# Kernel optimization log

Hardware: AMD Instinct MI355X
Metric: run time of the kernel (lower is better)

Reference implementation:

```python
import jax, jax.numpy as jnp
import numpy as np

INPUT_SIZE = 8
WINDOW = 128
HIDDEN = 256
B, T = 1024, 256

def _cell(W_ih, W_hh, b_ih, b_hh, h, c, x):
    # PyTorch LSTM gate order: i, f, g, o
    gates = x @ W_ih.T + h @ W_hh.T + b_ih + b_hh  # [B, 4H]
    i, f, g, o = jnp.split(gates, 4, axis=-1)
    c = jax.nn.sigmoid(f) * c + jax.nn.sigmoid(i) * jnp.tanh(g)
    h = jax.nn.sigmoid(o) * jnp.tanh(c)
    return h, c

def setup_inputs() -> dict:
    key = jax.random.key(0)
    ks = jax.random.split(key, 12)
    s = 1.0 / np.sqrt(HIDDEN)
    u = lambda k, shape: jax.random.uniform(k, shape, jnp.float32, -s, s)
    return {
        'x': jax.random.normal(ks[0], (B, T, INPUT_SIZE), jnp.float32),
        'W_ih0': u(ks[1], (4 * HIDDEN, INPUT_SIZE)),
        'W_hh0': u(ks[2], (4 * HIDDEN, HIDDEN)),
        'b_ih0': u(ks[3], (4 * HIDDEN,)),
        'b_hh0': u(ks[4], (4 * HIDDEN,)),
        'W_ih1': u(ks[5], (4 * HIDDEN, HIDDEN)),
        'W_hh1': u(ks[6], (4 * HIDDEN, HIDDEN)),
        'b_ih1': u(ks[7], (4 * HIDDEN,)),
        'b_hh1': u(ks[8], (4 * HIDDEN,)),
        'W_lin': u(ks[9], (1, HIDDEN)),
        'b_lin': u(ks[10], (1,)),
    }

def reference(x, W_ih0, W_hh0, b_ih0, b_hh0, W_ih1, W_hh1, b_ih1, b_hh1, W_lin, b_lin):
    Bx = x.shape[0]
    h0 = jnp.zeros((Bx, HIDDEN), x.dtype)
    params = [(W_ih0, W_hh0, b_ih0, b_hh0), (W_ih1, W_hh1, b_ih1, b_hh1)]

    # ---- warmup: multi-layer LSTM over first WINDOW steps ----
    x_pre = jnp.swapaxes(x[:, :WINDOW], 0, 1)   # [W, B, in]
    x_post = jnp.swapaxes(x[:, WINDOW:, 1:], 0, 1)  # [T-W, B, in-1]

    hs, cs = [], []
    seq = x_pre
    for (Wi, Wh, bi, bh) in params:
        def step(carry, xt, Wi=Wi, Wh=Wh, bi=bi, bh=bh):
            h, c = carry
            h, c = _cell(Wi, Wh, bi, bh, h, c, xt)
            return (h, c), h
        (hT, cT), seq = jax.lax.scan(step, (h0, h0), seq)
        hs.append(hT); cs.append(cT)

    pred0 = hs[-1] @ W_lin.T + b_lin  # [B, 1]

    def ar_step(carry, xt_rest):
        h0_, c0_, h1_, c1_, pred = carry
        xin = jnp.concatenate([pred, xt_rest], axis=1)  # [B, in]
        h0_, c0_ = _cell(W_ih0, W_hh0, b_ih0, b_hh0, h0_, c0_, xin)
        h1_, c1_ = _cell(W_ih1, W_hh1, b_ih1, b_hh1, h1_, c1_, h0_)
        pred = h1_ @ W_lin.T + b_lin
        return (h0_, c0_, h1_, c1_, pred), pred

    carry0 = (hs[0], cs[0], hs[1], cs[1], pred0)
    _, preds = jax.lax.scan(ar_step, carry0, x_post)  # [T-W, B, 1]

    out = jnp.concatenate([pred0[None], preds], axis=0)  # [T-W+1, B, 1]
    return jnp.swapaxes(out, 0, 1)  # [B, T-W+1, 1]
```

## Files before the change

kernel.cpp:

```cpp
#include <hip/hip_runtime.h>
#include <cstdint>

#define HID 256
#define TT 256
#define WIN 128
#define OUTW 129
#define NBLK 64
#define ROWS 16
#define NTHR 1024
#define NKK 25
#define NE (NKK * 64 * 512)

typedef _Float16 half8 __attribute__((ext_vector_type(8)));
typedef _Float16 half4 __attribute__((ext_vector_type(4)));
typedef float f32x4 __attribute__((ext_vector_type(4)));
typedef int i32x4 __attribute__((ext_vector_type(4)));

#define ALO  4.8828125e-4f
#define SLOC 1.5018521e-8f

__device__ __forceinline__ float sigm(float z)  { return 1.0f / (1.0f + __expf(-z)); }
__device__ __forceinline__ float tanhx(float z) { float e = __expf(2.0f * z); return 1.0f - 2.0f / (e + 1.0f); }

__device__ __forceinline__ void split_f(float v, _Float16& hi, _Float16& lo) {
  float h = (fabsf(v) < 0.0009765625f) ? 0.0f : (float)(_Float16)v;
  hi = (_Float16)h;
  lo = (_Float16)((v - h) * 2048.0f);
}
__device__ __forceinline__ signed char q8(float v) {
  return (signed char)__float2int_rn(fminf(fmaxf(v * 32.0f, -127.0f), 127.0f));
}

__global__ void prep_pack(const float* __restrict__ Wih0, const float* __restrict__ Whh0,
                          const float* __restrict__ Wih1, const float* __restrict__ Whh1,
                          _Float16* __restrict__ wpH, signed char* __restrict__ wpI) {
  for (int e = blockIdx.x * blockDim.x + threadIdx.x; e < NE; e += gridDim.x * blockDim.x) {
    const int kkG = e >> 15;
    const int nt = (e >> 9) & 63, l = (e >> 3) & 63, j = e & 7;
    const int kl = ((l >> 4) << 3) + j;
    const int n  = (nt << 4) + (l & 15);
    float w;
    if (kkG == 0)     w = (kl < 8) ? Wih0[n * 8 + kl] : 0.0f;
    else if (kkG < 9) w = Whh0[n * 256 + (kkG - 1) * 32 + kl];
    else {
      const int k = (kkG - 9) * 32 + kl;
      w = (k < 256) ? Wih1[n * 256 + k] : Whh1[n * 256 + (k - 256)];
    }
    const float hi = (fabsf(w) < 6.103515625e-5f) ? 0.0f : (float)(_Float16)w;
    wpH[e] = (_Float16)hi;
    int q = __float2int_rn((w - hi) * 2080768.0f);
    q = q > 127 ? 127 : (q < -127 ? -127 : q);
    wpI[e] = (signed char)q;
  }
}

__device__ __forceinline__ void mfma_kk(
    const _Float16* __restrict__ wpH, const signed char* __restrict__ wpI,
    int kkG, int w, int lane,
    const _Float16* __restrict__ ahp, const _Float16* __restrict__ alp,
    const signed char* __restrict__ aip,
    f32x4 (&accM)[4], f32x4 (&accA)[4], i32x4 (&accI)[4])
{
  const half8 ah = *(const half8*)ahp;
  const half8 al = *(const half8*)alp;
  const long  a8 = *(const long*)aip;
  const size_t b0 = ((size_t)kkG * 64 + w) * 512 + (size_t)lane * 8;
  #pragma unroll
  for (int i = 0; i < 4; ++i) {
    const half8 bh = *(const half8*)(wpH + b0 + (size_t)(i << 4) * 512);
    const long  b8 = *(const long*)(wpI + b0 + (size_t)(i << 4) * 512);
    accM[i] = __builtin_amdgcn_mfma_f32_16x16x32_f16(ah, bh, accM[i], 0, 0, 0);
    accA[i] = __builtin_amdgcn_mfma_f32_16x16x32_f16(al, bh, accA[i], 0, 0, 0);
    accI[i] = __builtin_amdgcn_mfma_i32_16x16x32_i8(a8, b8, accI[i], 0, 0, 0);
  }
}

__device__ __forceinline__ void epi(
    f32x4 (&accM)[4], f32x4 (&accA)[4], i32x4 (&accI)[4],
    float bi, float bf, float bg, float bo, float (&cst)[4],
    _Float16* __restrict__ Ah, _Float16* __restrict__ Al, signed char* __restrict__ Ai,
    int e0)
{
  #pragma unroll
  for (int q = 0; q < 4; ++q) {
    const float gi = accM[0][q] + ALO * accA[0][q] + SLOC * (float)accI[0][q] + bi;
    const float gf = accM[1][q] + ALO * accA[1][q] + SLOC * (float)accI[1][q] + bf;
    const float gg = accM[2][q] + ALO * accA[2][q] + SLOC * (float)accI[2][q] + bg;
    const float go = accM[3][q] + ALO * accA[3][q] + SLOC * (float)accI[3][q] + bo;
    const float c = sigm(gf) * cst[q] + sigm(gi) * tanhx(gg);
    cst[q] = c;
    const float h = sigm(go) * tanhx(c);
    _Float16 hh, hl; split_f(h, hh, hl);
    const int idx = e0 + (q << 3);
    Ah[idx] = hh; Al[idx] = hl; Ai[idx] = q8(h);
  }
}

__global__ __launch_bounds__(NTHR, 4) void lstm_mfma(
    const float* __restrict__ x,
    const float* __restrict__ bih0, const float* __restrict__ bhh0,
    const float* __restrict__ bih1, const float* __restrict__ bhh1,
    const float* __restrict__ Wlin, const float* __restrict__ blin,
    const _Float16* __restrict__ wpH, const signed char* __restrict__ wpI,
    float* __restrict__ out)
{
  __shared__ __align__(16) _Float16 A1h[8192];
  __shared__ __align__(16) _Float16 A1l[8192];
  __shared__ __align__(16) signed char A1i[8192];
  __shared__ __align__(16) _Float16 A0xh[512];
  __shared__ __align__(16) _Float16 A0xl[512];
  __shared__ __align__(16) signed char A0xi[512];
  __shared__ __align__(16) float sWlin[256];

  const int tid = threadIdx.x, lane = tid & 63, w = tid >> 6;
  const int r0 = blockIdx.x * ROWS;
  const int u = (w << 4) + (lane & 15);
  const int e0 = (((u >> 5) << 6) + (((u >> 3) & 3) << 4) + (((lane >> 4)) << 2)) * 8 + (u & 7);

  for (int i = tid; i < 8192; i += NTHR) { A1h[i] = (_Float16)0.f; A1l[i] = (_Float16)0.f; A1i[i] = 0; }
  if (tid < 512) { A0xh[tid] = (_Float16)0.f; A0xl[tid] = (_Float16)0.f; A0xi[tid] = 0; }
  if (tid < 256) sWlin[tid] = Wlin[tid];

  const float b0i = bih0[u]       + bhh0[u];
  const float b0f = bih0[u + 256] + bhh0[u + 256];
  const float b0g = bih0[u + 512] + bhh0[u + 512];
  const float b0o = bih0[u + 768] + bhh0[u + 768];
  const float b1i = bih1[u]       + bhh1[u];
  const float b1f = bih1[u + 256] + bhh1[u + 256];
  const float b1g = bih1[u + 512] + bhh1[u + 512];
  const float b1o = bih1[u + 768] + bhh1[u + 768];
  const float blv = blin[0];
  float c0[4] = {0.f, 0.f, 0.f, 0.f}, c1[4] = {0.f, 0.f, 0.f, 0.f};
  __syncthreads();

  for (int t = 0; t < TT; ++t) {
    if (t >= WIN) {
      const int u0 = lane << 2;
      const int pb = ((8 + (u0 >> 5)) * 64 + (((u0 >> 3) & 3) << 4) + w) * 8 + (u0 & 7);
      const half4 h4 = *(const half4*)(A1h + pb);
      const half4 l4 = *(const half4*)(A1l + pb);
      const float4 wl = *(const float4*)(sWlin + u0);
      float s = wl.x * ((float)h4.x + ALO * (float)l4.x)
              + wl.y * ((float)h4.y + ALO * (float)l4.y)
              + wl.z * ((float)h4.z + ALO * (float)l4.z)
              + wl.w * ((float)h4.w + ALO * (float)l4.w);
      #pragma unroll
      for (int m = 1; m < 64; m <<= 1) s += __shfl_xor(s, m);
      if (lane == 0) {
        const float pv = s + blv;
        out[(size_t)(r0 + w) * OUTW + (t - WIN)] = pv;
        _Float16 hh, hl; split_f(pv, hh, hl);
        A0xh[w << 3] = hh; A0xl[w << 3] = hl; A0xi[w << 3] = q8(pv);
      }
    }
    if (tid < 128) {
      const int r = tid >> 3, f = tid & 7;
      if (f > 0 || t < WIN) {
        const float v = x[((size_t)(r0 + r) * TT + t) * 8 + f];
        _Float16 hh, hl; split_f(v, hh, hl);
        A0xh[(r << 3) + f] = hh; A0xl[(r << 3) + f] = hl; A0xi[(r << 3) + f] = q8(v);
      }
    }
    __syncthreads();

    {
      f32x4 z4 = {0.f, 0.f, 0.f, 0.f}; i32x4 zi = {0, 0, 0, 0};
      f32x4 accM[4] = {z4, z4, z4, z4}, accA[4] = {z4, z4, z4, z4};
      i32x4 accI[4] = {zi, zi, zi, zi};
      mfma_kk(wpH, wpI, 0, w, lane,
              A0xh + lane * 8, A0xl + lane * 8, A0xi + lane * 8, accM, accA, accI);
      #pragma unroll 4
      for (int c = 1; c < 9; ++c) {
        const int ao = ((c - 1) * 64 + lane) * 8;
        mfma_kk(wpH, wpI, c, w, lane, A1h + ao, A1l + ao, A1i + ao, accM, accA, accI);
      }
      __syncthreads();
      epi(accM, accA, accI, b0i, b0f, b0g, b0o, c0, A1h, A1l, A1i, e0);
    }
    __syncthreads();

    {
      f32x4 z4 = {0.f, 0.f, 0.f, 0.f}; i32x4 zi = {0, 0, 0, 0};
      f32x4 accM[4] = {z4, z4, z4, z4}, accA[4] = {z4, z4, z4, z4};
      i32x4 accI[4] = {zi, zi, zi, zi};
      #pragma unroll 4
      for (int c = 0; c < 16; ++c) {
        const int ao = (c * 64 + lane) * 8;
        mfma_kk(wpH, wpI, 9 + c, w, lane, A1h + ao, A1l + ao, A1i + ao, accM, accA, accI);
      }
      __syncthreads();
      epi(accM, accA, accI, b1i, b1f, b1g, b1o, c1, A1h + 4096, A1l + 4096, A1i + 4096, e0);
    }
    __syncthreads();
  }

  {
    const int u0 = lane << 2;
    const int pb = ((8 + (u0 >> 5)) * 64 + (((u0 >> 3) & 3) << 4) + w) * 8 + (u0 & 7);
    const half4 h4 = *(const half4*)(A1h + pb);
    const half4 l4 = *(const half4*)(A1l + pb);
    const float4 wl = *(const float4*)(sWlin + u0);
    float s = wl.x * ((float)h4.x + ALO * (float)l4.x)
            + wl.y * ((float)h4.y + ALO * (float)l4.y)
            + wl.z * ((float)h4.z + ALO * (float)l4.z)
            + wl.w * ((float)h4.w + ALO * (float)l4.w);
    #pragma unroll
    for (int m = 1; m < 64; m <<= 1) s += __shfl_xor(s, m);
    if (lane == 0) out[(size_t)(r0 + w) * OUTW + 128] = s + blv;
  }
}

extern "C" void kernel_launch(void* const* d_in, const int* in_sizes, int n_in,
                              void* d_out, int out_size, void* d_ws, size_t ws_size,
                              hipStream_t stream) {
  (void)in_sizes; (void)n_in; (void)out_size; (void)ws_size;
  const float* x    = (const float*)d_in[0];
  const float* Wih0 = (const float*)d_in[1];
  const float* Whh0 = (const float*)d_in[2];
  const float* bih0 = (const float*)d_in[3];
  const float* bhh0 = (const float*)d_in[4];
  const float* Wih1 = (const float*)d_in[5];
  const float* Whh1 = (const float*)d_in[6];
  const float* bih1 = (const float*)d_in[7];
  const float* bhh1 = (const float*)d_in[8];
  const float* Wlin = (const float*)d_in[9];
  const float* blin = (const float*)d_in[10];
  _Float16* wpH   = (_Float16*)d_ws;
  signed char* wpI = (signed char*)d_ws + (size_t)NE * 2;
  float* out = (float*)d_out;

  prep_pack<<<1600, 256, 0, stream>>>(Wih0, Whh0, Wih1, Whh1, wpH, wpI);
  lstm_mfma<<<NBLK, NTHR, 0, stream>>>(x, bih0, bhh0, bih1, bhh1,
                                       Wlin, blin, wpH, wpI, out);
}
```

Measured before the change: 12.25 ms.

## Stream packed weights into LDS with async global_load_lds double buffering

Each step's weight tiles, which were loaded straight from global memory into registers, are now staged through a two-slot LDS buffer using global_load_lds. Manual vmcnt and lgkmcnt waits let the next unit's prefetch overlap the current MFMAs, and a continuous unit schedule runs across both layers and timesteps. The int8 residual weights are repacked so each lane reads two tiles' worth in one 16-byte load. The kernel now needs about 140KB of dynamic LDS and relies on hand-counted waitcnt, which is fragile if the compiler reorders memory operations.

```diff
diff --git a/kernel.cpp b/kernel.cpp
--- a/kernel.cpp
+++ b/kernel.cpp
@@ -10,14 +10,33 @@
 #define NTHR 1024
 #define NKK 25
 #define NE (NKK * 64 * 512)
+#define NP (NKK * 32 * 64 * 16)
 
 typedef _Float16 half8 __attribute__((ext_vector_type(8)));
 typedef _Float16 half4 __attribute__((ext_vector_type(4)));
 typedef float f32x4 __attribute__((ext_vector_type(4)));
 typedef int i32x4 __attribute__((ext_vector_type(4)));
+typedef long l2v __attribute__((ext_vector_type(2)));
 
 #define ALO  4.8828125e-4f
 #define SLOC 1.5018521e-8f
+
+#define B_HALF   49152
+#define OFF_A1H  98304
+#define OFF_A1L  114688
+#define OFF_A1I  131072
+#define OFF_A0XH 139264
+#define OFF_A0XL 140288
+#define OFF_A0XI 141312
+#define OFF_WLIN 141824
+#define SMEM_BYTES 142848
+
+#define VMWAIT3() asm volatile("s_waitcnt vmcnt(3)" ::: "memory")
+#define LGKM0()   asm volatile("s_waitcnt lgkmcnt(0)" ::: "memory")
+#define BAR()     { LGKM0(); __builtin_amdgcn_s_barrier(); asm volatile("" ::: "memory"); }
+
+#define MF16(a,b,c) __builtin_amdgcn_mfma_f32_16x16x32_f16(a,b,c,0,0,0)
+#define MI8(a,b,c)  __builtin_amdgcn_mfma_i32_16x16x32_i8(a,b,c,0,0,0)
 
 __device__ __forceinline__ float sigm(float z)  { return 1.0f / (1.0f + __expf(-z)); }
 __device__ __forceinline__ float tanhx(float z) { float e = __expf(2.0f * z); return 1.0f - 2.0f / (e + 1.0f); }
@@ -31,48 +50,64 @@
   return (signed char)__float2int_rn(fminf(fmaxf(v * 32.0f, -127.0f), 127.0f));
 }
 
+__device__ __forceinline__ void gload16(const void* g, void* l) {
+  __builtin_amdgcn_global_load_lds(
+      (const __attribute__((address_space(1))) void*)g,
+      (__attribute__((address_space(3))) void*)l, 16, 0, 0);
+}
+
+__device__ __forceinline__ float fetch_w(int kkG, int kl, int n,
+    const float* __restrict__ Wih0, const float* __restrict__ Whh0,
+    const float* __restrict__ Wih1, const float* __restrict__ Whh1) {
+  if (kkG == 0) return (kl < 8) ? Wih0[n * 8 + kl] : 0.0f;
+  if (kkG < 9)  return Whh0[n * 256 + (kkG - 1) * 32 + kl];
+  const int k = (kkG - 9) * 32 + kl;
+  return (k < 256) ? Wih1[n * 256 + k] : Whh1[n * 256 + (k - 256)];
+}
+
 __global__ void prep_pack(const float* __restrict__ Wih0, const float* __restrict__ Whh0,
                           const float* __restrict__ Wih1, const float* __restrict__ Whh1,
-                          _Float16* __restrict__ wpH, signed char* __restrict__ wpI) {
-  for (int e = blockIdx.x * blockDim.x + threadIdx.x; e < NE; e += gridDim.x * blockDim.x) {
+                          _Float16* __restrict__ wpH, unsigned char* __restrict__ wpP) {
+  const int stride = gridDim.x * blockDim.x;
+  for (int e = blockIdx.x * blockDim.x + threadIdx.x; e < NE; e += stride) {
     const int kkG = e >> 15;
     const int nt = (e >> 9) & 63, l = (e >> 3) & 63, j = e & 7;
     const int kl = ((l >> 4) << 3) + j;
     const int n  = (nt << 4) + (l & 15);
-    float w;
-    if (kkG == 0)     w = (kl < 8) ? Wih0[n * 8 + kl] : 0.0f;
-    else if (kkG < 9) w = Whh0[n * 256 + (kkG - 1) * 32 + kl];
-    else {
-      const int k = (kkG - 9) * 32 + kl;
-      w = (k < 256) ? Wih1[n * 256 + k] : Whh1[n * 256 + (k - 256)];
-    }
+    const float w = fetch_w(kkG, kl, n, Wih0, Whh0, Wih1, Whh1);
     const float hi = (fabsf(w) < 6.103515625e-5f) ? 0.0f : (float)(_Float16)w;
     wpH[e] = (_Float16)hi;
+  }
+  for (int e = blockIdx.x * blockDim.x + threadIdx.x; e < NP; e += stride) {
+    const int kkG = e >> 15;
+    const int rem = e & 32767;
+    const int pair = rem >> 10;
+    const int l = (rem >> 4) & 63;
+    const int b = rem & 15;
+    const int tilesel = b >> 3, j = b & 7;
+    const int nt = ((pair >> 4) << 5) + (pair & 15) + (tilesel << 4);
+    const int kl = ((l >> 4) << 3) + j;
+    const int n  = (nt << 4) + (l & 15);
+    const float w = fetch_w(kkG, kl, n, Wih0, Whh0, Wih1, Whh1);
+    const float hi = (fabsf(w) < 6.103515625e-5f) ? 0.0f : (float)(_Float16)w;
     int q = __float2int_rn((w - hi) * 2080768.0f);
     q = q > 127 ? 127 : (q < -127 ? -127 : q);
-    wpI[e] = (signed char)q;
-  }
-}
-
-__device__ __forceinline__ void mfma_kk(
-    const _Float16* __restrict__ wpH, const signed char* __restrict__ wpI,
-    int kkG, int w, int lane,
-    const _Float16* __restrict__ ahp, const _Float16* __restrict__ alp,
-    const signed char* __restrict__ aip,
-    f32x4 (&accM)[4], f32x4 (&accA)[4], i32x4 (&accI)[4])
-{
-  const half8 ah = *(const half8*)ahp;
-  const half8 al = *(const half8*)alp;
-  const long  a8 = *(const long*)aip;
-  const size_t b0 = ((size_t)kkG * 64 + w) * 512 + (size_t)lane * 8;
-  #pragma unroll
-  for (int i = 0; i < 4; ++i) {
-    const half8 bh = *(const half8*)(wpH + b0 + (size_t)(i << 4) * 512);
-    const long  b8 = *(const long*)(wpI + b0 + (size_t)(i << 4) * 512);
-    accM[i] = __builtin_amdgcn_mfma_f32_16x16x32_f16(ah, bh, accM[i], 0, 0, 0);
-    accA[i] = __builtin_amdgcn_mfma_f32_16x16x32_f16(al, bh, accA[i], 0, 0, 0);
-    accI[i] = __builtin_amdgcn_mfma_i32_16x16x32_i8(a8, b8, accI[i], 0, 0, 0);
-  }
+    wpP[e] = (unsigned char)(signed char)q;
+  }
+}
+
+__device__ __forceinline__ void stage_unit(int u, int w, int lane,
+    const _Float16* __restrict__ wpH, const unsigned char* __restrict__ wpP,
+    char* __restrict__ sB) {
+  const int kkG  = (u < 18) ? (u >> 1) : (9 + ((u - 18) >> 1));
+  const int half = u & 1;
+  const int nt0  = (half << 5) + w;
+  char* dst = sB + (half ? B_HALF : 0) + w * 3072;
+  const char* sH0 = (const char*)(wpH + (((size_t)(kkG << 6) + nt0) << 9)) + (lane << 4);
+  const char* sP  = (const char*)wpP + (((size_t)(kkG << 5) + (half << 4) + w) << 10) + (lane << 4);
+  gload16(sH0,          dst);
+  gload16(sH0 + 16384,  dst + 1024);
+  gload16(sP,           dst + 2048);
 }
 
 __device__ __forceinline__ void epi(
@@ -101,21 +136,23 @@
     const float* __restrict__ bih0, const float* __restrict__ bhh0,
     const float* __restrict__ bih1, const float* __restrict__ bhh1,
     const float* __restrict__ Wlin, const float* __restrict__ blin,
-    const _Float16* __restrict__ wpH, const signed char* __restrict__ wpI,
+    const _Float16* __restrict__ wpH, const unsigned char* __restrict__ wpP,
     float* __restrict__ out)
 {
-  __shared__ __align__(16) _Float16 A1h[8192];
-  __shared__ __align__(16) _Float16 A1l[8192];
-  __shared__ __align__(16) signed char A1i[8192];
-  __shared__ __align__(16) _Float16 A0xh[512];
-  __shared__ __align__(16) _Float16 A0xl[512];
-  __shared__ __align__(16) signed char A0xi[512];
-  __shared__ __align__(16) float sWlin[256];
+  extern __shared__ char sm[];
+  char* sB = sm;
+  _Float16*    A1h  = (_Float16*)(sm + OFF_A1H);
+  _Float16*    A1l  = (_Float16*)(sm + OFF_A1L);
+  signed char* A1i  = (signed char*)(sm + OFF_A1I);
+  _Float16*    A0xh = (_Float16*)(sm + OFF_A0XH);
+  _Float16*    A0xl = (_Float16*)(sm + OFF_A0XL);
+  signed char* A0xi = (signed char*)(sm + OFF_A0XI);
+  float*       sWlin = (float*)(sm + OFF_WLIN);
 
   const int tid = threadIdx.x, lane = tid & 63, w = tid >> 6;
   const int r0 = blockIdx.x * ROWS;
   const int u = (w << 4) + (lane & 15);
-  const int e0 = (((u >> 5) << 6) + (((u >> 3) & 3) << 4) + (((lane >> 4)) << 2)) * 8 + (u & 7);
+  const int e0 = (((u >> 5) << 6) + (((u >> 3) & 3) << 4) + ((lane >> 4) << 2)) * 8 + (u & 7);
 
   for (int i = tid; i < 8192; i += NTHR) { A1h[i] = (_Float16)0.f; A1l[i] = (_Float16)0.f; A1i[i] = 0; }
   if (tid < 512) { A0xh[tid] = (_Float16)0.f; A0xl[tid] = (_Float16)0.f; A0xi[tid] = 0; }
@@ -131,7 +168,10 @@
   const float b1o = bih1[u + 768] + bhh1[u + 768];
   const float blv = blin[0];
   float c0[4] = {0.f, 0.f, 0.f, 0.f}, c1[4] = {0.f, 0.f, 0.f, 0.f};
-  __syncthreads();
+  BAR();
+
+  stage_unit(0, w, lane, wpH, wpP, sB);
+  stage_unit(1, w, lane, wpH, wpP, sB);
 
   for (int t = 0; t < TT; ++t) {
     if (t >= WIN) {
@@ -161,37 +201,93 @@
         A0xh[(r << 3) + f] = hh; A0xl[(r << 3) + f] = hl; A0xi[(r << 3) + f] = q8(v);
       }
     }
-    __syncthreads();
+    BAR();
 
     {
       f32x4 z4 = {0.f, 0.f, 0.f, 0.f}; i32x4 zi = {0, 0, 0, 0};
       f32x4 accM[4] = {z4, z4, z4, z4}, accA[4] = {z4, z4, z4, z4};
       i32x4 accI[4] = {zi, zi, zi, zi};
-      mfma_kk(wpH, wpI, 0, w, lane,
-              A0xh + lane * 8, A0xl + lane * 8, A0xi + lane * 8, accM, accA, accI);
-      #pragma unroll 4
-      for (int c = 1; c < 9; ++c) {
-        const int ao = ((c - 1) * 64 + lane) * 8;
-        mfma_kk(wpH, wpI, c, w, lane, A1h + ao, A1l + ao, A1i + ao, accM, accA, accI);
+      half8 ah, al; long a8;
+      #pragma unroll
+      for (int c = 0; c < 9; ++c) {
+        {
+          const char* mb = sB + w * 3072;
+          VMWAIT3();
+          const half8 bh0 = *(const half8*)(mb + (lane << 4));
+          const half8 bh1 = *(const half8*)(mb + 1024 + (lane << 4));
+          const l2v pp    = *(const l2v*)(mb + 2048 + (lane << 4));
+          if (c == 0) {
+            ah = *(const half8*)(A0xh + (lane << 3));
+            al = *(const half8*)(A0xl + (lane << 3));
+            a8 = *(const long*)(A0xi + (lane << 3));
+          } else {
+            const int ao = (((c - 1) << 6) + lane) << 3;
+            ah = *(const half8*)(A1h + ao);
+            al = *(const half8*)(A1l + ao);
+            a8 = *(const long*)(A1i + ao);
+          }
+          LGKM0();
+          stage_unit(2 * c + 2, w, lane, wpH, wpP, sB);
+          accM[0] = MF16(ah, bh0, accM[0]); accA[0] = MF16(al, bh0, accA[0]); accI[0] = MI8(a8, pp[0], accI[0]);
+          accM[1] = MF16(ah, bh1, accM[1]); accA[1] = MF16(al, bh1, accA[1]); accI[1] = MI8(a8, pp[1], accI[1]);
+        }
+        {
+          const char* mb = sB + B_HALF + w * 3072;
+          VMWAIT3();
+          const half8 bh0 = *(const half8*)(mb + (lane << 4));
+          const half8 bh1 = *(const half8*)(mb + 1024 + (lane << 4));
+          const l2v pp    = *(const l2v*)(mb + 2048 + (lane << 4));
+          LGKM0();
+          stage_unit(2 * c + 3, w, lane, wpH, wpP, sB);
+          accM[2] = MF16(ah, bh0, accM[2]); accA[2] = MF16(al, bh0, accA[2]); accI[2] = MI8(a8, pp[0], accI[2]);
+          accM[3] = MF16(ah, bh1, accM[3]); accA[3] = MF16(al, bh1, accA[3]); accI[3] = MI8(a8, pp[1], accI[3]);
+        }
       }
-      __syncthreads();
+      BAR();
       epi(accM, accA, accI, b0i, b0f, b0g, b0o, c0, A1h, A1l, A1i, e0);
     }
-    __syncthreads();
+    BAR();
 
     {
       f32x4 z4 = {0.f, 0.f, 0.f, 0.f}; i32x4 zi = {0, 0, 0, 0};
       f32x4 accM[4] = {z4, z4, z4, z4}, accA[4] = {z4, z4, z4, z4};
       i32x4 accI[4] = {zi, zi, zi, zi};
-      #pragma unroll 4
+      half8 ah, al; long a8;
+      #pragma unroll
       for (int c = 0; c < 16; ++c) {
-        const int ao = (c * 64 + lane) * 8;
-        mfma_kk(wpH, wpI, 9 + c, w, lane, A1h + ao, A1l + ao, A1i + ao, accM, accA, accI);
+        {
+          const char* mb = sB + w * 3072;
+          VMWAIT3();
+          const half8 bh0 = *(const half8*)(mb + (lane << 4));
+          const half8 bh1 = *(const half8*)(mb + 1024 + (lane << 4));
+          const l2v pp    = *(const l2v*)(mb + 2048 + (lane << 4));
+          const int ao = ((c << 6) + lane) << 3;
+          ah = *(const half8*)(A1h + ao);
+          al = *(const half8*)(A1l + ao);
+          a8 = *(const long*)(A1i + ao);
+          LGKM0();
+          const int uu = (20 + 2 * c >= 50) ? (20 + 2 * c - 50) : (20 + 2 * c);
+          stage_unit(uu, w, lane, wpH, wpP, sB);
+          accM[0] = MF16(ah, bh0, accM[0]); accA[0] = MF16(al, bh0, accA[0]); accI[0] = MI8(a8, pp[0], accI[0]);
+          accM[1] = MF16(ah, bh1, accM[1]); accA[1] = MF16(al, bh1, accA[1]); accI[1] = MI8(a8, pp[1], accI[1]);
+        }
+        {
+          const char* mb = sB + B_HALF + w * 3072;
+          VMWAIT3();
+          const half8 bh0 = *(const half8*)(mb + (lane << 4));
+          const half8 bh1 = *(const half8*)(mb + 1024 + (lane << 4));
+          const l2v pp    = *(const l2v*)(mb + 2048 + (lane << 4));
+          LGKM0();
+          const int uu = (21 + 2 * c >= 50) ? (21 + 2 * c - 50) : (21 + 2 * c);
+          stage_unit(uu, w, lane, wpH, wpP, sB);
+          accM[2] = MF16(ah, bh0, accM[2]); accA[2] = MF16(al, bh0, accA[2]); accI[2] = MI8(a8, pp[0], accI[2]);
+          accM[3] = MF16(ah, bh1, accM[3]); accA[3] = MF16(al, bh1, accA[3]); accI[3] = MI8(a8, pp[1], accI[3]);
+        }
       }
-      __syncthreads();
+      BAR();
       epi(accM, accA, accI, b1i, b1f, b1g, b1o, c1, A1h + 4096, A1l + 4096, A1i + 4096, e0);
     }
-    __syncthreads();
+    BAR();
   }
 
   {
@@ -225,11 +321,14 @@
   const float* bhh1 = (const float*)d_in[8];
   const float* Wlin = (const float*)d_in[9];
   const float* blin = (const float*)d_in[10];
-  _Float16* wpH   = (_Float16*)d_ws;
-  signed char* wpI = (signed char*)d_ws + (size_t)NE * 2;
+  _Float16* wpH     = (_Float16*)d_ws;
+  unsigned char* wpP = (unsigned char*)d_ws + (size_t)NE * 2;
   float* out = (float*)d_out;
 
-  prep_pack<<<1600, 256, 0, stream>>>(Wih0, Whh0, Wih1, Whh1, wpH, wpI);
-  lstm_mfma<<<NBLK, NTHR, 0, stream>>>(x, bih0, bhh0, bih1, bhh1,
-                                       Wlin, blin, wpH, wpI, out);
-}
+  prep_pack<<<1600, 256, 0, stream>>>(Wih0, Whh0, Wih1, Whh1, wpH, wpP);
+
+  (void)hipFuncSetAttribute(reinterpret_cast<const void*>(lstm_mfma),
+                            hipFuncAttributeMaxDynamicSharedMemorySize, SMEM_BYTES);
+  lstm_mfma<<<NBLK, NTHR, SMEM_BYTES, stream>>>(x, bih0, bhh0, bih1, bhh1,
+                                                Wlin, blin, wpH, wpP, out);
+}
```

Result: slower. 18.09 ms (+47.7%).

## Replace fp16 split-precision MFMA with multi-plane int8 MFMA emulation

Applied to the files above, without the earlier changes.

Switches the recurrent matmuls from fp16 hi/lo plus int8 correction MFMAs to a pure int8 scheme: weights are split into two int8 planes and hidden states into three int8 planes, combined with five i8 MFMAs per tile and scaled in the epilogue. The input projection for layer 0 (8 features) moves out of the MFMA path into per-thread fp32 FMAs using register-held weights, dropping one K-chunk. The final hidden state is also kept in fp32 shared memory for the linear head. This targets the higher throughput and smaller operand footprint of int8 MFMA, but raises the MFMA count per tile and may affect accuracy through the quantization.

```diff
diff --git a/kernel.cpp b/kernel.cpp
--- a/kernel.cpp
+++ b/kernel.cpp
@@ -8,202 +8,233 @@
 #define NBLK 64
 #define ROWS 16
 #define NTHR 1024
-#define NKK 25
-#define NE (NKK * 64 * 512)
-
-typedef _Float16 half8 __attribute__((ext_vector_type(8)));
-typedef _Float16 half4 __attribute__((ext_vector_type(4)));
+#define NKK 24
+#define PLANE_B (NKK * 32 * 64 * 16)
+
 typedef float f32x4 __attribute__((ext_vector_type(4)));
 typedef int i32x4 __attribute__((ext_vector_type(4)));
-
-#define ALO  4.8828125e-4f
-#define SLOC 1.5018521e-8f
+typedef long l2v __attribute__((ext_vector_type(2)));
+
+#define S1Q  4.9212598e-4f
+#define S0C  3.8750078e-6f
+#define C1   3.93700787e-3f
+#define C2   1.55000310e-5f
+#define R127 7.874015748e-3f
+#define R32258 3.10000620e-5f
+
+#define MI8(a,b,c) __builtin_amdgcn_mfma_i32_16x16x32_i8(a,b,c,0,0,0)
 
 __device__ __forceinline__ float sigm(float z)  { return 1.0f / (1.0f + __expf(-z)); }
 __device__ __forceinline__ float tanhx(float z) { float e = __expf(2.0f * z); return 1.0f - 2.0f / (e + 1.0f); }
 
-__device__ __forceinline__ void split_f(float v, _Float16& hi, _Float16& lo) {
-  float h = (fabsf(v) < 0.0009765625f) ? 0.0f : (float)(_Float16)v;
-  hi = (_Float16)h;
-  lo = (_Float16)((v - h) * 2048.0f);
-}
-__device__ __forceinline__ signed char q8(float v) {
-  return (signed char)__float2int_rn(fminf(fmaxf(v * 32.0f, -127.0f), 127.0f));
-}
-
-__global__ void prep_pack(const float* __restrict__ Wih0, const float* __restrict__ Whh0,
-                          const float* __restrict__ Wih1, const float* __restrict__ Whh1,
-                          _Float16* __restrict__ wpH, signed char* __restrict__ wpI) {
-  for (int e = blockIdx.x * blockDim.x + threadIdx.x; e < NE; e += gridDim.x * blockDim.x) {
+__device__ __forceinline__ int clamp127(int v) { return v > 127 ? 127 : (v < -127 ? -127 : v); }
+
+__device__ __forceinline__ void enc_h(float h, signed char& qh, signed char& ql, signed char& qll) {
+  float e = h;
+  int a = __float2int_rn(e * 127.0f);
+  e = fmaf((float)(-a), R127, e);
+  int b = clamp127(__float2int_rn(e * 32258.0f));
+  e = fmaf((float)(-b), R32258, e);
+  int c = clamp127(__float2int_rn(e * 8193532.0f));
+  qh = (signed char)a; ql = (signed char)b; qll = (signed char)c;
+}
+
+__global__ void prep_pack(const float* __restrict__ Whh0, const float* __restrict__ Wih1,
+                          const float* __restrict__ Whh1,
+                          signed char* __restrict__ wpHi, signed char* __restrict__ wpLo) {
+  const int stride = gridDim.x * blockDim.x;
+  for (int e = blockIdx.x * blockDim.x + threadIdx.x; e < PLANE_B; e += stride) {
     const int kkG = e >> 15;
-    const int nt = (e >> 9) & 63, l = (e >> 3) & 63, j = e & 7;
-    const int kl = ((l >> 4) << 3) + j;
+    const int rem = e & 32767;
+    const int p = rem >> 10;
+    const int l = (rem >> 4) & 63;
+    const int b = rem & 15;
+    const int tilesel = b >> 3, j = b & 7;
+    const int nt = (p & 15) + ((p >> 4) << 5) + (tilesel << 4);
     const int n  = (nt << 4) + (l & 15);
+    const int kl = ((kkG & 7) << 5) + ((l >> 4) << 3) + j;
     float w;
-    if (kkG == 0)     w = (kl < 8) ? Wih0[n * 8 + kl] : 0.0f;
-    else if (kkG < 9) w = Whh0[n * 256 + (kkG - 1) * 32 + kl];
-    else {
-      const int k = (kkG - 9) * 32 + kl;
-      w = (k < 256) ? Wih1[n * 256 + k] : Whh1[n * 256 + (k - 256)];
-    }
-    const float hi = (fabsf(w) < 6.103515625e-5f) ? 0.0f : (float)(_Float16)w;
-    wpH[e] = (_Float16)hi;
-    int q = __float2int_rn((w - hi) * 2080768.0f);
-    q = q > 127 ? 127 : (q < -127 ? -127 : q);
-    wpI[e] = (signed char)q;
-  }
-}
-
-__device__ __forceinline__ void mfma_kk(
-    const _Float16* __restrict__ wpH, const signed char* __restrict__ wpI,
-    int kkG, int w, int lane,
-    const _Float16* __restrict__ ahp, const _Float16* __restrict__ alp,
-    const signed char* __restrict__ aip,
-    f32x4 (&accM)[4], f32x4 (&accA)[4], i32x4 (&accI)[4])
-{
-  const half8 ah = *(const half8*)ahp;
-  const half8 al = *(const half8*)alp;
-  const long  a8 = *(const long*)aip;
-  const size_t b0 = ((size_t)kkG * 64 + w) * 512 + (size_t)lane * 8;
-  #pragma unroll
-  for (int i = 0; i < 4; ++i) {
-    const half8 bh = *(const half8*)(wpH + b0 + (size_t)(i << 4) * 512);
-    const long  b8 = *(const long*)(wpI + b0 + (size_t)(i << 4) * 512);
-    accM[i] = __builtin_amdgcn_mfma_f32_16x16x32_f16(ah, bh, accM[i], 0, 0, 0);
-    accA[i] = __builtin_amdgcn_mfma_f32_16x16x32_f16(al, bh, accA[i], 0, 0, 0);
-    accI[i] = __builtin_amdgcn_mfma_i32_16x16x32_i8(a8, b8, accI[i], 0, 0, 0);
-  }
-}
-
-__device__ __forceinline__ void epi(
-    f32x4 (&accM)[4], f32x4 (&accA)[4], i32x4 (&accI)[4],
-    float bi, float bf, float bg, float bo, float (&cst)[4],
-    _Float16* __restrict__ Ah, _Float16* __restrict__ Al, signed char* __restrict__ Ai,
-    int e0)
-{
-  #pragma unroll
-  for (int q = 0; q < 4; ++q) {
-    const float gi = accM[0][q] + ALO * accA[0][q] + SLOC * (float)accI[0][q] + bi;
-    const float gf = accM[1][q] + ALO * accA[1][q] + SLOC * (float)accI[1][q] + bf;
-    const float gg = accM[2][q] + ALO * accA[2][q] + SLOC * (float)accI[2][q] + bg;
-    const float go = accM[3][q] + ALO * accA[3][q] + SLOC * (float)accI[3][q] + bo;
-    const float c = sigm(gf) * cst[q] + sigm(gi) * tanhx(gg);
-    cst[q] = c;
-    const float h = sigm(go) * tanhx(c);
-    _Float16 hh, hl; split_f(h, hh, hl);
-    const int idx = e0 + (q << 3);
-    Ah[idx] = hh; Al[idx] = hl; Ai[idx] = q8(h);
-  }
-}
-
-__global__ __launch_bounds__(NTHR, 4) void lstm_mfma(
+    if (kkG < 8)       w = Whh0[n * 256 + kl];
+    else if (kkG < 16) w = Wih1[n * 256 + kl];
+    else               w = Whh1[n * 256 + kl];
+    const int qh = clamp127(__float2int_rn(w * 2032.0f));
+    const float resid = fmaf((float)(-qh), S1Q, w);
+    const int ql = clamp127(__float2int_rn(resid * 516128.0f));
+    wpHi[e] = (signed char)qh;
+    wpLo[e] = (signed char)ql;
+  }
+}
+
+__global__ __launch_bounds__(NTHR) void lstm_i8(
     const float* __restrict__ x,
     const float* __restrict__ bih0, const float* __restrict__ bhh0,
     const float* __restrict__ bih1, const float* __restrict__ bhh1,
-    const float* __restrict__ Wlin, const float* __restrict__ blin,
-    const _Float16* __restrict__ wpH, const signed char* __restrict__ wpI,
+    const float* __restrict__ Wih0, const float* __restrict__ Wlin,
+    const float* __restrict__ blin,
+    const signed char* __restrict__ wpHi, const signed char* __restrict__ wpLo,
     float* __restrict__ out)
 {
-  __shared__ __align__(16) _Float16 A1h[8192];
-  __shared__ __align__(16) _Float16 A1l[8192];
-  __shared__ __align__(16) signed char A1i[8192];
-  __shared__ __align__(16) _Float16 A0xh[512];
-  __shared__ __align__(16) _Float16 A0xl[512];
-  __shared__ __align__(16) signed char A0xi[512];
-  __shared__ __align__(16) float sWlin[256];
+  __shared__ __align__(8) signed char aH[8192];
+  __shared__ __align__(8) signed char aL[8192];
+  __shared__ __align__(8) signed char aLL[8192];
+  __shared__ float sH1[4096];
+  __shared__ float xf[128];
+  __shared__ float sWlin[256];
 
   const int tid = threadIdx.x, lane = tid & 63, w = tid >> 6;
   const int r0 = blockIdx.x * ROWS;
   const int u = (w << 4) + (lane & 15);
-  const int e0 = (((u >> 5) << 6) + (((u >> 3) & 3) << 4) + (((lane >> 4)) << 2)) * 8 + (u & 7);
-
-  for (int i = tid; i < 8192; i += NTHR) { A1h[i] = (_Float16)0.f; A1l[i] = (_Float16)0.f; A1i[i] = 0; }
-  if (tid < 512) { A0xh[tid] = (_Float16)0.f; A0xl[tid] = (_Float16)0.f; A0xi[tid] = 0; }
+  const int dr0 = (lane >> 4) << 2;
+  const int e0 = (((u >> 5) << 6) + (((u >> 3) & 3) << 4) + dr0) * 8 + (u & 7);
+
+  for (int i = tid; i < 2048; i += NTHR) {
+    ((int*)aH)[i] = 0; ((int*)aL)[i] = 0; ((int*)aLL)[i] = 0;
+  }
+  for (int i = tid; i < 4096; i += NTHR) sH1[i] = 0.0f;
+  if (tid < 128) xf[tid] = 0.0f;
   if (tid < 256) sWlin[tid] = Wlin[tid];
 
-  const float b0i = bih0[u]       + bhh0[u];
-  const float b0f = bih0[u + 256] + bhh0[u + 256];
-  const float b0g = bih0[u + 512] + bhh0[u + 512];
-  const float b0o = bih0[u + 768] + bhh0[u + 768];
-  const float b1i = bih1[u]       + bhh1[u];
-  const float b1f = bih1[u + 256] + bhh1[u + 256];
-  const float b1g = bih1[u + 512] + bhh1[u + 512];
-  const float b1o = bih1[u + 768] + bhh1[u + 768];
+  float wxr[8][4];
+  float b0v[4], b1v[4];
+  #pragma unroll
+  for (int i = 0; i < 4; ++i) {
+    const int n = (i << 8) + u;
+    b0v[i] = bih0[n] + bhh0[n];
+    b1v[i] = bih1[n] + bhh1[n];
+    #pragma unroll
+    for (int f = 0; f < 8; ++f) wxr[f][i] = Wih0[n * 8 + f];
+  }
   const float blv = blin[0];
   float c0[4] = {0.f, 0.f, 0.f, 0.f}, c1[4] = {0.f, 0.f, 0.f, 0.f};
   __syncthreads();
 
   for (int t = 0; t < TT; ++t) {
     if (t >= WIN) {
-      const int u0 = lane << 2;
-      const int pb = ((8 + (u0 >> 5)) * 64 + (((u0 >> 3) & 3) << 4) + w) * 8 + (u0 & 7);
-      const half4 h4 = *(const half4*)(A1h + pb);
-      const half4 l4 = *(const half4*)(A1l + pb);
-      const float4 wl = *(const float4*)(sWlin + u0);
-      float s = wl.x * ((float)h4.x + ALO * (float)l4.x)
-              + wl.y * ((float)h4.y + ALO * (float)l4.y)
-              + wl.z * ((float)h4.z + ALO * (float)l4.z)
-              + wl.w * ((float)h4.w + ALO * (float)l4.w);
+      const int n0 = lane << 2;
+      const float4 wl = *(const float4*)(sWlin + n0);
+      const float4 h4 = *(const float4*)(sH1 + (w << 8) + n0);
+      float s = wl.x * h4.x + wl.y * h4.y + wl.z * h4.z + wl.w * h4.w;
       #pragma unroll
       for (int m = 1; m < 64; m <<= 1) s += __shfl_xor(s, m);
       if (lane == 0) {
         const float pv = s + blv;
         out[(size_t)(r0 + w) * OUTW + (t - WIN)] = pv;
-        _Float16 hh, hl; split_f(pv, hh, hl);
-        A0xh[w << 3] = hh; A0xl[w << 3] = hl; A0xi[w << 3] = q8(pv);
+        xf[w] = pv;
       }
     }
     if (tid < 128) {
       const int r = tid >> 3, f = tid & 7;
-      if (f > 0 || t < WIN) {
-        const float v = x[((size_t)(r0 + r) * TT + t) * 8 + f];
-        _Float16 hh, hl; split_f(v, hh, hl);
-        A0xh[(r << 3) + f] = hh; A0xl[(r << 3) + f] = hl; A0xi[(r << 3) + f] = q8(v);
-      }
+      if (f > 0 || t < WIN)
+        xf[(f << 4) + r] = x[((size_t)(r0 + r) * TT + t) * 8 + f];
     }
     __syncthreads();
 
     {
-      f32x4 z4 = {0.f, 0.f, 0.f, 0.f}; i32x4 zi = {0, 0, 0, 0};
-      f32x4 accM[4] = {z4, z4, z4, z4}, accA[4] = {z4, z4, z4, z4};
-      i32x4 accI[4] = {zi, zi, zi, zi};
-      mfma_kk(wpH, wpI, 0, w, lane,
-              A0xh + lane * 8, A0xl + lane * 8, A0xi + lane * 8, accM, accA, accI);
-      #pragma unroll 4
-      for (int c = 1; c < 9; ++c) {
-        const int ao = ((c - 1) * 64 + lane) * 8;
-        mfma_kk(wpH, wpI, c, w, lane, A1h + ao, A1l + ao, A1i + ao, accM, accA, accI);
+      f32x4 g0[4];
+      #pragma unroll
+      for (int i = 0; i < 4; ++i) { g0[i][0] = b0v[i]; g0[i][1] = b0v[i]; g0[i][2] = b0v[i]; g0[i][3] = b0v[i]; }
+      #pragma unroll
+      for (int f = 0; f < 8; ++f) {
+        float xq0 = xf[(f << 4) + dr0], xq1 = xf[(f << 4) + dr0 + 1];
+        float xq2 = xf[(f << 4) + dr0 + 2], xq3 = xf[(f << 4) + dr0 + 3];
+        #pragma unroll
+        for (int i = 0; i < 4; ++i) {
+          g0[i][0] = fmaf(wxr[f][i], xq0, g0[i][0]);
+          g0[i][1] = fmaf(wxr[f][i], xq1, g0[i][1]);
+          g0[i][2] = fmaf(wxr[f][i], xq2, g0[i][2]);
+          g0[i][3] = fmaf(wxr[f][i], xq3, g0[i][3]);
+        }
+      }
+      i32x4 zi = {0, 0, 0, 0};
+      i32x4 acc0[4] = {zi, zi, zi, zi}, acc1[4] = {zi, zi, zi, zi}, acc2[4] = {zi, zi, zi, zi};
+      #pragma unroll
+      for (int c = 0; c < 8; ++c) {
+        const int ao = ((c << 6) + lane) << 3;
+        const long a0 = *(const long*)(aH + ao);
+        const long a1 = *(const long*)(aL + ao);
+        const long a2 = *(const long*)(aLL + ao);
+        const size_t bo = ((((size_t)(c << 5) + w) << 6) + lane) << 4;
+        const l2v hA = *(const l2v*)(wpHi + bo);
+        const l2v hB = *(const l2v*)(wpHi + bo + 16384);
+        const l2v lA = *(const l2v*)(wpLo + bo);
+        const l2v lB = *(const l2v*)(wpLo + bo + 16384);
+        const long bh[4] = {hA[0], hA[1], hB[0], hB[1]};
+        const long bl[4] = {lA[0], lA[1], lB[0], lB[1]};
+        #pragma unroll
+        for (int i = 0; i < 4; ++i) {
+          acc0[i] = MI8(a0, bh[i], acc0[i]);
+          acc1[i] = MI8(a1, bh[i], acc1[i]);
+          acc1[i] = MI8(a0, bl[i], acc1[i]);
+          acc2[i] = MI8(a2, bh[i], acc2[i]);
+          acc2[i] = MI8(a1, bl[i], acc2[i]);
+        }
       }
       __syncthreads();
-      epi(accM, accA, accI, b0i, b0f, b0g, b0o, c0, A1h, A1l, A1i, e0);
+      #pragma unroll
+      for (int q = 0; q < 4; ++q) {
+        const float gi = g0[0][q] + S0C * ((float)acc0[0][q] + C1 * (float)acc1[0][q] + C2 * (float)acc2[0][q]);
+        const float gf = g0[1][q] + S0C * ((float)acc0[1][q] + C1 * (float)acc1[1][q] + C2 * (float)acc2[1][q]);
+        const float gg = g0[2][q] + S0C * ((float)acc0[2][q] + C1 * (float)acc1[2][q] + C2 * (float)acc2[2][q]);
+        const float go = g0[3][q] + S0C * ((float)acc0[3][q] + C1 * (float)acc1[3][q] + C2 * (float)acc2[3][q]);
+        const float c = sigm(gf) * c0[q] + sigm(gi) * tanhx(gg);
+        c0[q] = c;
+        const float h = sigm(go) * tanhx(c);
+        signed char qh, ql, qll; enc_h(h, qh, ql, qll);
+        const int idx = e0 + (q << 3);
+        aH[idx] = qh; aL[idx] = ql; aLL[idx] = qll;
+      }
     }
     __syncthreads();
 
     {
-      f32x4 z4 = {0.f, 0.f, 0.f, 0.f}; i32x4 zi = {0, 0, 0, 0};
-      f32x4 accM[4] = {z4, z4, z4, z4}, accA[4] = {z4, z4, z4, z4};
-      i32x4 accI[4] = {zi, zi, zi, zi};
-      #pragma unroll 4
+      i32x4 zi = {0, 0, 0, 0};
+      i32x4 acc0[4] = {zi, zi, zi, zi}, acc1[4] = {zi, zi, zi, zi}, acc2[4] = {zi, zi, zi, zi};
+      #pragma unroll
       for (int c = 0; c < 16; ++c) {
-        const int ao = (c * 64 + lane) * 8;
-        mfma_kk(wpH, wpI, 9 + c, w, lane, A1h + ao, A1l + ao, A1i + ao, accM, accA, accI);
+        const int ao = ((c << 6) + lane) << 3;
+        const long a0 = *(const long*)(aH + ao);
+        const long a1 = *(const long*)(aL + ao);
+        const long a2 = *(const long*)(aLL + ao);
+        const size_t bo = ((((size_t)((8 + c) << 5) + w) << 6) + lane) << 4;
+        const l2v hA = *(const l2v*)(wpHi + bo);
+        const l2v hB = *(const l2v*)(wpHi + bo + 16384);
+        const l2v lA = *(const l2v*)(wpLo + bo);
+        const l2v lB = *(const l2v*)(wpLo + bo + 16384);
+        const long bh[4] = {hA[0], hA[1], hB[0], hB[1]};
+        const long bl[4] = {lA[0], lA[1], lB[0], lB[1]};
+        #pragma unroll
+        for (int i = 0; i < 4; ++i) {
+          acc0[i] = MI8(a0, bh[i], acc0[i]);
+          acc1[i] = MI8(a1, bh[i], acc1[i]);
+          acc1[i] = MI8(a0, bl[i], acc1[i]);
+          acc2[i] = MI8(a2, bh[i], acc2[i]);
+          acc2[i] = MI8(a1, bl[i], acc2[i]);
+        }
       }
       __syncthreads();
-      epi(accM, accA, accI, b1i, b1f, b1g, b1o, c1, A1h + 4096, A1l + 4096, A1i + 4096, e0);
+      #pragma unroll
+      for (int q = 0; q < 4; ++q) {
+        const float gi = b1v[0] + S0C * ((float)acc0[0][q] + C1 * (float)acc1[0][q] + C2 * (float)acc2[0][q]);
+        const float gf = b1v[1] + S0C * ((float)acc0[1][q] + C1 * (float)acc1[1][q] + C2 * (float)acc2[1][q]);
+        const float gg = b1v[2] + S0C * ((float)acc0[2][q] + C1 * (float)acc1[2][q] + C2 * (float)acc2[2][q]);
+        const float go = b1v[3] + S0C * ((float)acc0[3][q] + C1 * (float)acc1[3][q] + C2 * (float)acc2[3][q]);
+        const float c = sigm(gf) * c1[q] + sigm(gi) * tanhx(gg);
+        c1[q] = c;
+        const float h = sigm(go) * tanhx(c);
+        signed char qh, ql, qll; enc_h(h, qh, ql, qll);
+        const int idx = 4096 + e0 + (q << 3);
+        aH[idx] = qh; aL[idx] = ql; aLL[idx] = qll;
+        sH1[((dr0 + q) << 8) + u] = h;
+      }
     }
     __syncthreads();
   }
 
   {
-    const int u0 = lane << 2;
-    const int pb = ((8 + (u0 >> 5)) * 64 + (((u0 >> 3) & 3) << 4) + w) * 8 + (u0 & 7);
-    const half4 h4 = *(const half4*)(A1h + pb);
-    const half4 l4 = *(const half4*)(A1l + pb);
-    const float4 wl = *(const float4*)(sWlin + u0);
-    float s = wl.x * ((float)h4.x + ALO * (float)l4.x)
-            + wl.y * ((float)h4.y + ALO * (float)l4.y)
-            + wl.z * ((float)h4.z + ALO * (float)l4.z)
-            + wl.w * ((float)h4.w + ALO * (float)l4.w);
+    const int n0 = lane << 2;
+    const float4 wl = *(const float4*)(sWlin + n0);
+    const float4 h4 = *(const float4*)(sH1 + (w << 8) + n0);
+    float s = wl.x * h4.x + wl.y * h4.y + wl.z * h4.z + wl.w * h4.w;
     #pragma unroll
     for (int m = 1; m < 64; m <<= 1) s += __shfl_xor(s, m);
     if (lane == 0) out[(size_t)(r0 + w) * OUTW + 128] = s + blv;
@@ -225,11 +256,11 @@
   const float* bhh1 = (const float*)d_in[8];
   const float* Wlin = (const float*)d_in[9];
   const float* blin = (const float*)d_in[10];
-  _Float16* wpH   = (_Float16*)d_ws;
-  signed char* wpI = (signed char*)d_ws + (size_t)NE * 2;
+  signed char* wpHi = (signed char*)d_ws;
+  signed char* wpLo = wpHi + PLANE_B;
   float* out = (float*)d_out;
 
-  prep_pack<<<1600, 256, 0, stream>>>(Wih0, Whh0, Wih1, Whh1, wpH, wpI);
-  lstm_mfma<<<NBLK, NTHR, 0, stream>>>(x, bih0, bhh0, bih1, bhh1,
-                                       Wlin, blin, wpH, wpI, out);
-}
+  prep_pack<<<1536, 256, 0, stream>>>(Whh0, Wih1, Whh1, wpHi, wpLo);
+  lstm_i8<<<NBLK, NTHR, 0, stream>>>(x, bih0, bhh0, bih1, bhh1,
+                                     Wih0, Wlin, blin, wpHi, wpLo, out);
+}
```

Result: slower. 15.21 ms (+24.2%).
